# Kernel optimization log

Hardware: AMD Instinct MI355X
Metric: run time of the kernel (lower is better)

## Reference

```python
import jax, jax.numpy as jnp
import numpy as np

B, N, DIM = 8, 1024, 512
HEADS, DIM_HEAD = 8, 64
INNER = HEADS * DIM_HEAD  # 512
SCALE = DIM_HEAD ** -0.5
EPS = 1e-5


def setup_inputs() -> dict:
    key = jax.random.key(0)
    k = jax.random.split(key, 6)
    x = jax.random.normal(k[0], (B, N, DIM), dtype=jnp.float32)
    gamma = jnp.ones((DIM,), dtype=jnp.float32)
    beta = jnp.zeros((DIM,), dtype=jnp.float32)
    # Linear weights stored as (in, out) so y = x @ W (equivalent to torch x @ W.T)
    W_qk = jax.random.normal(k[1], (DIM, 2 * INNER), dtype=jnp.float32) * (DIM ** -0.5)
    W_v = jax.random.normal(k[2], (DIM, INNER), dtype=jnp.float32) * (DIM ** -0.5)
    W_out = jax.random.normal(k[3], (INNER, DIM), dtype=jnp.float32) * (INNER ** -0.5)
    return {"x": x, "gamma": gamma, "beta": beta, "W_qk": W_qk, "W_v": W_v, "W_out": W_out}


def _layernorm(x, gamma, beta):
    mu = jnp.mean(x, axis=-1, keepdims=True)
    var = jnp.mean(jnp.square(x - mu), axis=-1, keepdims=True)
    return (x - mu) * jax.lax.rsqrt(var + EPS) * gamma + beta


def reference(x, gamma, beta, W_qk, W_v, W_out):
    xn = _layernorm(x, gamma, beta)                       # [B,N,D]
    v = xn @ W_v                                          # [B,N,INNER]
    qk = xn @ W_qk                                        # [B,N,2*INNER]
    q, k = jnp.split(qk, 2, axis=-1)
    # b n (h d) -> b h n d
    q = q.reshape(B, N, HEADS, DIM_HEAD).transpose(0, 2, 1, 3)
    k = k.reshape(B, N, HEADS, DIM_HEAD).transpose(0, 2, 1, 3)
    vh = v.reshape(B, N, HEADS, DIM_HEAD).transpose(0, 2, 1, 3)
    dots = jnp.einsum('bhnd,bhmd->bhnm', q, k) * SCALE    # [B,H,N,N]
    attn = jax.nn.softmax(dots, axis=-1)
    out = jnp.einsum('bhnm,bhmd->bhnd', attn, vh)         # [B,H,N,d]
    out = out.transpose(0, 2, 1, 3).reshape(B, N, INNER)  # b h n d -> b n (h d)
    return out @ W_out                                    # [B,N,DIM]
```

## Files before the change

### kernel.cpp

```cpp
#include <hip/hip_runtime.h>

#define TOK 8192
#define DMODEL 512
#define SEQ 1024
#define NH 8
#define DH 64

typedef _Float16 half8 __attribute__((ext_vector_type(8)));
typedef _Float16 half4v __attribute__((ext_vector_type(4)));
typedef float floatx4 __attribute__((ext_vector_type(4)));

__device__ __forceinline__ void gll16(const void* g, void* l) {
  __builtin_amdgcn_global_load_lds(
      (const __attribute__((address_space(1))) void*)g,
      (__attribute__((address_space(3))) void*)l, 16, 0, 0);
}

__global__ __launch_bounds__(256) void ln_kernel(
    const float* __restrict__ x, const float* __restrict__ gamma,
    const float* __restrict__ beta, _Float16* __restrict__ xn) {
  const int row = blockIdx.x * 4 + (threadIdx.x >> 6);
  const int t = threadIdx.x & 63;
  const float* xr = x + (size_t)row * DMODEL;
  const float4 a = *(const float4*)(xr + t * 4);
  const float4 b = *(const float4*)(xr + 256 + t * 4);
  float s  = a.x + a.y + a.z + a.w + b.x + b.y + b.z + b.w;
  float ss = a.x*a.x + a.y*a.y + a.z*a.z + a.w*a.w
           + b.x*b.x + b.y*b.y + b.z*b.z + b.w*b.w;
  #pragma unroll
  for (int m = 1; m < 64; m <<= 1) {
    s  += __shfl_xor(s, m);
    ss += __shfl_xor(ss, m);
  }
  const float mean = s * (1.0f / DMODEL);
  const float var  = ss * (1.0f / DMODEL) - mean * mean;
  const float inv  = rsqrtf(var + 1e-5f);
  const float4 g0  = *(const float4*)(gamma + t * 4);
  const float4 g1  = *(const float4*)(gamma + 256 + t * 4);
  const float4 be0 = *(const float4*)(beta + t * 4);
  const float4 be1 = *(const float4*)(beta + 256 + t * 4);
  half4v o0, o1;
  o0[0] = (_Float16)((a.x - mean) * inv * g0.x + be0.x);
  o0[1] = (_Float16)((a.y - mean) * inv * g0.y + be0.y);
  o0[2] = (_Float16)((a.z - mean) * inv * g0.z + be0.z);
  o0[3] = (_Float16)((a.w - mean) * inv * g0.w + be0.w);
  o1[0] = (_Float16)((b.x - mean) * inv * g1.x + be1.x);
  o1[1] = (_Float16)((b.y - mean) * inv * g1.y + be1.y);
  o1[2] = (_Float16)((b.z - mean) * inv * g1.z + be1.z);
  o1[3] = (_Float16)((b.w - mean) * inv * g1.w + be1.w);
  _Float16* outr = xn + (size_t)row * DMODEL;
  *(half4v*)(outr + t * 4) = o0;
  *(half4v*)(outr + 256 + t * 4) = o1;
}

__global__ __launch_bounds__(256) void transpose_cvt3_kernel(
    const float* __restrict__ Wqk, const float* __restrict__ Wv,
    const float* __restrict__ Wo, _Float16* __restrict__ WqkvT,
    _Float16* __restrict__ WoutT) {
  const int z = blockIdx.z;
  const float* W;
  _Float16* dst;
  int N, rowoff;
  if (z == 0)      { W = Wqk; dst = WqkvT; N = 1024; rowoff = 0; }
  else if (z == 1) { W = Wv;  dst = WqkvT; N = 512;  rowoff = 1024; }
  else             { W = Wo;  dst = WoutT; N = 512;  rowoff = 0; }
  const int n0 = blockIdx.x * 32;
  if (n0 >= N) return;
  const int k0 = blockIdx.y * 32;
  __shared__ float t[32][33];
  const int tx = threadIdx.x & 31, ty = threadIdx.x >> 5;
  #pragma unroll
  for (int j = 0; j < 4; ++j)
    t[ty + j * 8][tx] = W[(size_t)(k0 + ty + j * 8) * N + n0 + tx];
  __syncthreads();
  #pragma unroll
  for (int j = 0; j < 4; ++j)
    dst[(size_t)(rowoff + n0 + ty + j * 8) * 512 + k0 + tx] =
        (_Float16)t[tx][ty + j * 8];
}

template <int MODE>
__global__ __launch_bounds__(256) void hgemm_kernel(
    const _Float16* __restrict__ A, const _Float16* __restrict__ Bt,
    void* __restrict__ Cout, void* __restrict__ Cout2, int M, int N, int K) {
  __shared__ char smem[65536];
  const int tid = threadIdx.x;
  const int bm = blockIdx.x, bn = blockIdx.y;
  const int wv = tid >> 6, lane = tid & 63;
  const int l15 = lane & 15, g = lane >> 4;
  const int wr = wv >> 1, wc = wv & 1;
  const int swz = (l15 & 7) << 4;
  const _Float16* Ab = A + (size_t)(bm * 128) * K;
  const _Float16* Bb = Bt + (size_t)(bn * 128) * K;
  const int lrow = lane >> 3;
  const int lchk = (lane & 7) * 16;
  const int ssw = lchk ^ (lrow << 4);

  #define HG_STAGE(buf, kt)                                                  \
    _Pragma("unroll")                                                        \
    for (int i = 0; i < 4; ++i) {                                            \
      const int row = wv * 32 + i * 8 + lrow;                                \
      gll16((const char*)(Ab + (size_t)row * K + (kt)) + ssw,                \
            smem + (buf) * 32768 + (wv * 32 + i * 8) * 128);                 \
      gll16((const char*)(Bb + (size_t)row * K + (kt)) + ssw,                \
            smem + (buf) * 32768 + 16384 + (wv * 32 + i * 8) * 128);         \
    }

  floatx4 acc[4][4] = {};
  HG_STAGE(0, 0);
  __syncthreads();
  int cur = 0;
  for (int kt = 0; kt < K; kt += 64) {
    if (kt + 64 < K) { HG_STAGE(cur ^ 1, kt + 64); }
    const char* sb = smem + cur * 32768;
    #pragma unroll
    for (int kk = 0; kk < 2; ++kk) {
      half8 af[4], bf[4];
      #pragma unroll
      for (int mt = 0; mt < 4; ++mt)
        af[mt] = *(const half8*)(sb + (wr * 64 + mt * 16 + l15) * 128 +
                                 ((g * 16 + kk * 64) ^ swz));
      #pragma unroll
      for (int nt = 0; nt < 4; ++nt)
        bf[nt] = *(const half8*)(sb + 16384 + (wc * 64 + nt * 16 + l15) * 128 +
                                 ((g * 16 + kk * 64) ^ swz));
      #pragma unroll
      for (int mt = 0; mt < 4; ++mt)
        #pragma unroll
        for (int nt = 0; nt < 4; ++nt)
          acc[mt][nt] = __builtin_amdgcn_mfma_f32_16x16x32_f16(
              af[mt], bf[nt], acc[mt][nt], 0, 0, 0);
    }
    __syncthreads();
    cur ^= 1;
  }
  #undef HG_STAGE
  const int m0 = bm * 128 + wr * 64;
  const int n0 = bn * 128 + wc * 64;
  if constexpr (MODE == 0) {
    float* C = (float*)Cout;
    #pragma unroll
    for (int mt = 0; mt < 4; ++mt)
      #pragma unroll
      for (int nt = 0; nt < 4; ++nt) {
        const int n = n0 + nt * 16 + l15;
        #pragma unroll
        for (int r = 0; r < 4; ++r)
          C[(size_t)(m0 + mt * 16 + 4 * g + r) * 512 + n] = acc[mt][nt][r];
      }
  } else {
    _Float16* Q = (_Float16*)Cout;
    _Float16* V = (_Float16*)Cout2;
    #pragma unroll
    for (int mt = 0; mt < 4; ++mt) {
      const int mrow = m0 + mt * 16 + 4 * g;
      const int b = mrow >> 10, tok = mrow & 1023;
      #pragma unroll
      for (int nt = 0; nt < 4; ++nt) {
        const int n = n0 + nt * 16 + l15;
        if (n < 1024) {
          #pragma unroll
          for (int r = 0; r < 4; ++r)
            Q[(size_t)(mrow + r) * 1024 + n] = (_Float16)acc[mt][nt][r];
        } else {
          const int cv = n - 1024;
          half4v hv;
          #pragma unroll
          for (int r = 0; r < 4; ++r) hv[r] = (_Float16)acc[mt][nt][r];
          *(half4v*)(V + ((size_t)((b * 8 + (cv >> 6)) * 64 + (cv & 63)) << 10) + tok) = hv;
        }
      }
    }
  }
}

#define QSC 0.18033688f
#define MOFF 5.7707801f

__global__ __launch_bounds__(512) void flash16_kernel(
    const _Float16* __restrict__ qkh, const _Float16* __restrict__ vt,
    _Float16* __restrict__ ao) {
  __shared__ char smem[65536];
  const int bh = blockIdx.x;
  const int qt = blockIdx.y;
  const int b = bh >> 3, h = bh & 7;
  const int tid = threadIdx.x;
  const int wv = tid >> 6, lane = tid & 63;
  const int l15 = lane & 15, g = lane >> 4;
  const int swz = (l15 & 7) << 4;
  const int qrow0 = b * SEQ + qt * 128;

  half8 qf[2];
  {
    const _Float16* qp = qkh + (size_t)(qrow0 + wv * 16 + l15) * 1024 + h * DH;
    qf[0] = *(const half8*)(qp + g * 8);
    qf[1] = *(const half8*)(qp + g * 8 + 32);
    qf[0] *= (_Float16)QSC;
    qf[1] *= (_Float16)QSC;
  }

  float lsum = 0.f;
  floatx4 oacc[4] = {};

  const int lrow = lane >> 3;
  const int lchk = (lane & 7) * 16;
  const int ssw = lchk ^ (lrow << 4);
  const _Float16* kbase = qkh + 512 + h * DH;
  const _Float16* vbase = vt + (size_t)bh * 64 * 1024;
  char* pb = smem + 49152 + wv * 2048 + l15 * 128;

  #define FL_STAGE(buf, kt)                                                   \
    {                                                                         \
      const int krow = b * SEQ + (kt) * 64 + wv * 8 + lrow;                   \
      gll16((const char*)(kbase + (size_t)krow * 1024) + ssw,                 \
            smem + (buf) * 16384 + wv * 1024);                                \
      gll16((const char*)(vbase + (size_t)(wv * 8 + lrow) * 1024 +            \
                          (kt) * 64) + ssw,                                   \
            smem + (buf) * 16384 + 8192 + wv * 1024);                         \
    }

  FL_STAGE(0, 0);
  FL_STAGE(1, 1);
  int cur = 0;
  for (int kt = 0; kt < 16; ++kt) {
    if (kt < 15) asm volatile("s_waitcnt vmcnt(2)" ::: "memory");
    else         asm volatile("s_waitcnt vmcnt(0)" ::: "memory");
    __builtin_amdgcn_s_barrier();
    asm volatile("" ::: "memory");
    const int nxt = cur + 2 >= 3 ? cur - 1 : cur + 2;
    if (kt + 2 < 16) FL_STAGE(nxt, kt + 2);
    const char* sb = smem + cur * 16384;

    floatx4 sacc[4] = {};
    __builtin_amdgcn_s_setprio(1);
    #pragma unroll
    for (int kk = 0; kk < 2; ++kk) {
      #pragma unroll
      for (int mt = 0; mt < 4; ++mt) {
        half8 af = *(const half8*)(sb + (16 * mt + l15) * 128 +
                                   ((g * 16 + kk * 64) ^ swz));
        sacc[mt] = __builtin_amdgcn_mfma_f32_16x16x32_f16(af, qf[kk], sacc[mt], 0, 0, 0);
      }
    }
    __builtin_amdgcn_s_setprio(0);

    float rs = 0.f;
    #pragma unroll
    for (int mt = 0; mt < 4; ++mt) {
      float p0 = exp2f(sacc[mt][0] - MOFF);
      float p1 = exp2f(sacc[mt][1] - MOFF);
      float p2 = exp2f(sacc[mt][2] - MOFF);
      float p3 = exp2f(sacc[mt][3] - MOFF);
      rs += (p0 + p1) + (p2 + p3);
      half4v pv;
      pv[0] = (_Float16)p0; pv[1] = (_Float16)p1;
      pv[2] = (_Float16)p2; pv[3] = (_Float16)p3;
      *(half4v*)(pb + ((32 * mt + 8 * g) ^ swz)) = pv;
    }
    rs += __shfl_xor(rs, 16);
    rs += __shfl_xor(rs, 32);
    lsum += rs;

    __builtin_amdgcn_s_setprio(1);
    #pragma unroll
    for (int kk = 0; kk < 2; ++kk) {
      half8 pf = *(const half8*)(pb + ((g * 16 + kk * 64) ^ swz));
      #pragma unroll
      for (int mt = 0; mt < 4; ++mt) {
        half8 vf = *(const half8*)(sb + 8192 + (16 * mt + l15) * 128 +
                                   ((g * 16 + kk * 64) ^ swz));
        oacc[mt] = __builtin_amdgcn_mfma_f32_16x16x32_f16(vf, pf, oacc[mt], 0, 0, 0);
      }
    }
    __builtin_amdgcn_s_setprio(0);
    cur = cur + 1 >= 3 ? 0 : cur + 1;
  }
  #undef FL_STAGE

  const float inv = 1.0f / lsum;
  _Float16* op = ao + (size_t)(qrow0 + wv * 16 + l15) * 512 + h * DH;
  #pragma unroll
  for (int mt = 0; mt < 4; ++mt) {
    half4v hv;
    hv[0] = (_Float16)(oacc[mt][0] * inv);
    hv[1] = (_Float16)(oacc[mt][1] * inv);
    hv[2] = (_Float16)(oacc[mt][2] * inv);
    hv[3] = (_Float16)(oacc[mt][3] * inv);
    *(half4v*)(op + 16 * mt + 4 * g) = hv;
  }
}

extern "C" void kernel_launch(void* const* d_in, const int* in_sizes, int n_in,
                              void* d_out, int out_size, void* d_ws, size_t ws_size,
                              hipStream_t stream) {
  const float* x     = (const float*)d_in[0];
  const float* gamma = (const float*)d_in[1];
  const float* beta  = (const float*)d_in[2];
  const float* W_qk  = (const float*)d_in[3];
  const float* W_v   = (const float*)d_in[4];
  const float* W_out = (const float*)d_in[5];
  float* out = (float*)d_out;
  char* ws = (char*)d_ws;

  const size_t MB = 1024 * 1024;
  _Float16* xn16  = (_Float16*)ws;
  _Float16* qkh   = (_Float16*)(ws + 8 * MB);
  _Float16* vt    = (_Float16*)(ws + 24 * MB);
  _Float16* ao16  = (_Float16*)(ws + 32 * MB);
  _Float16* WqkvT = (_Float16*)(ws + 40 * MB);
  _Float16* WoutT = (_Float16*)(ws + 42 * MB);

  transpose_cvt3_kernel<<<dim3(32, 16, 3), 256, 0, stream>>>(
      W_qk, W_v, W_out, WqkvT, WoutT);
  ln_kernel<<<TOK / 4, 256, 0, stream>>>(x, gamma, beta, xn16);
  hgemm_kernel<3><<<dim3(64, 12), 256, 0, stream>>>(
      xn16, WqkvT, qkh, vt, TOK, 1536, 512);
  flash16_kernel<<<dim3(64, 8), 512, 0, stream>>>(qkh, vt, ao16);
  hgemm_kernel<0><<<dim3(64, 4), 256, 0, stream>>>(
      ao16, WoutT, out, nullptr, TOK, 512, 512);
}
```

Baseline: 81.90 us.

## Merge LN and weight transpose kernels; triple-buffer GEMM with BK=32 pipeline

Merges the layernorm kernel and the weight transpose/convert kernel into one launch that picks its role from the block index, removing one kernel launch. Reworks the GEMM main loop from a double-buffered 64-wide K tile into a three-stage ring of 32-wide K tiles. Loads are issued two stages ahead and waited on with explicit vmcnt counts and a raw barrier, and MFMA priority is raised during compute. LDS drops to 48KB, which may allow more blocks per CU, at the cost of more barriers per K step and a new swizzle pattern.

```diff
diff --git a/kernel.cpp b/kernel.cpp
--- a/kernel.cpp
+++ b/kernel.cpp
@@ -16,123 +16,130 @@
       (__attribute__((address_space(3))) void*)l, 16, 0, 0);
 }
 
-__global__ __launch_bounds__(256) void ln_kernel(
+__global__ __launch_bounds__(256) void prep_kernel(
     const float* __restrict__ x, const float* __restrict__ gamma,
-    const float* __restrict__ beta, _Float16* __restrict__ xn) {
-  const int row = blockIdx.x * 4 + (threadIdx.x >> 6);
-  const int t = threadIdx.x & 63;
-  const float* xr = x + (size_t)row * DMODEL;
-  const float4 a = *(const float4*)(xr + t * 4);
-  const float4 b = *(const float4*)(xr + 256 + t * 4);
-  float s  = a.x + a.y + a.z + a.w + b.x + b.y + b.z + b.w;
-  float ss = a.x*a.x + a.y*a.y + a.z*a.z + a.w*a.w
-           + b.x*b.x + b.y*b.y + b.z*b.z + b.w*b.w;
-  #pragma unroll
-  for (int m = 1; m < 64; m <<= 1) {
-    s  += __shfl_xor(s, m);
-    ss += __shfl_xor(ss, m);
-  }
-  const float mean = s * (1.0f / DMODEL);
-  const float var  = ss * (1.0f / DMODEL) - mean * mean;
-  const float inv  = rsqrtf(var + 1e-5f);
-  const float4 g0  = *(const float4*)(gamma + t * 4);
-  const float4 g1  = *(const float4*)(gamma + 256 + t * 4);
-  const float4 be0 = *(const float4*)(beta + t * 4);
-  const float4 be1 = *(const float4*)(beta + 256 + t * 4);
-  half4v o0, o1;
-  o0[0] = (_Float16)((a.x - mean) * inv * g0.x + be0.x);
-  o0[1] = (_Float16)((a.y - mean) * inv * g0.y + be0.y);
-  o0[2] = (_Float16)((a.z - mean) * inv * g0.z + be0.z);
-  o0[3] = (_Float16)((a.w - mean) * inv * g0.w + be0.w);
-  o1[0] = (_Float16)((b.x - mean) * inv * g1.x + be1.x);
-  o1[1] = (_Float16)((b.y - mean) * inv * g1.y + be1.y);
-  o1[2] = (_Float16)((b.z - mean) * inv * g1.z + be1.z);
-  o1[3] = (_Float16)((b.w - mean) * inv * g1.w + be1.w);
-  _Float16* outr = xn + (size_t)row * DMODEL;
-  *(half4v*)(outr + t * 4) = o0;
-  *(half4v*)(outr + 256 + t * 4) = o1;
-}
-
-__global__ __launch_bounds__(256) void transpose_cvt3_kernel(
+    const float* __restrict__ beta, _Float16* __restrict__ xn,
     const float* __restrict__ Wqk, const float* __restrict__ Wv,
     const float* __restrict__ Wo, _Float16* __restrict__ WqkvT,
     _Float16* __restrict__ WoutT) {
-  const int z = blockIdx.z;
-  const float* W;
-  _Float16* dst;
-  int N, rowoff;
-  if (z == 0)      { W = Wqk; dst = WqkvT; N = 1024; rowoff = 0; }
-  else if (z == 1) { W = Wv;  dst = WqkvT; N = 512;  rowoff = 1024; }
-  else             { W = Wo;  dst = WoutT; N = 512;  rowoff = 0; }
-  const int n0 = blockIdx.x * 32;
-  if (n0 >= N) return;
-  const int k0 = blockIdx.y * 32;
   __shared__ float t[32][33];
-  const int tx = threadIdx.x & 31, ty = threadIdx.x >> 5;
-  #pragma unroll
-  for (int j = 0; j < 4; ++j)
-    t[ty + j * 8][tx] = W[(size_t)(k0 + ty + j * 8) * N + n0 + tx];
-  __syncthreads();
-  #pragma unroll
-  for (int j = 0; j < 4; ++j)
-    dst[(size_t)(rowoff + n0 + ty + j * 8) * 512 + k0 + tx] =
-        (_Float16)t[tx][ty + j * 8];
+  const int bid = blockIdx.x;
+  if (bid < 2048) {
+    const int row = bid * 4 + (threadIdx.x >> 6);
+    const int tt = threadIdx.x & 63;
+    const float* xr = x + (size_t)row * DMODEL;
+    const float4 a = *(const float4*)(xr + tt * 4);
+    const float4 b = *(const float4*)(xr + 256 + tt * 4);
+    float s  = a.x + a.y + a.z + a.w + b.x + b.y + b.z + b.w;
+    float ss = a.x*a.x + a.y*a.y + a.z*a.z + a.w*a.w
+             + b.x*b.x + b.y*b.y + b.z*b.z + b.w*b.w;
+    #pragma unroll
+    for (int m = 1; m < 64; m <<= 1) {
+      s  += __shfl_xor(s, m);
+      ss += __shfl_xor(ss, m);
+    }
+    const float mean = s * (1.0f / DMODEL);
+    const float var  = ss * (1.0f / DMODEL) - mean * mean;
+    const float inv  = rsqrtf(var + 1e-5f);
+    const float4 g0  = *(const float4*)(gamma + tt * 4);
+    const float4 g1  = *(const float4*)(gamma + 256 + tt * 4);
+    const float4 be0 = *(const float4*)(beta + tt * 4);
+    const float4 be1 = *(const float4*)(beta + 256 + tt * 4);
+    half4v o0, o1;
+    o0[0] = (_Float16)((a.x - mean) * inv * g0.x + be0.x);
+    o0[1] = (_Float16)((a.y - mean) * inv * g0.y + be0.y);
+    o0[2] = (_Float16)((a.z - mean) * inv * g0.z + be0.z);
+    o0[3] = (_Float16)((a.w - mean) * inv * g0.w + be0.w);
+    o1[0] = (_Float16)((b.x - mean) * inv * g1.x + be1.x);
+    o1[1] = (_Float16)((b.y - mean) * inv * g1.y + be1.y);
+    o1[2] = (_Float16)((b.z - mean) * inv * g1.z + be1.z);
+    o1[3] = (_Float16)((b.w - mean) * inv * g1.w + be1.w);
+    _Float16* outr = xn + (size_t)row * DMODEL;
+    *(half4v*)(outr + tt * 4) = o0;
+    *(half4v*)(outr + 256 + tt * 4) = o1;
+  } else {
+    const int r = bid - 2048;
+    const int z = r >> 9;
+    const int rem = r & 511;
+    const float* W;
+    _Float16* dst;
+    int N, rowoff;
+    if (z == 0)      { W = Wqk; dst = WqkvT; N = 1024; rowoff = 0; }
+    else if (z == 1) { W = Wv;  dst = WqkvT; N = 512;  rowoff = 1024; }
+    else             { W = Wo;  dst = WoutT; N = 512;  rowoff = 0; }
+    const int n0 = (rem & 31) * 32;
+    if (n0 >= N) return;
+    const int k0 = (rem >> 5) * 32;
+    const int tx = threadIdx.x & 31, ty = threadIdx.x >> 5;
+    #pragma unroll
+    for (int j = 0; j < 4; ++j)
+      t[ty + j * 8][tx] = W[(size_t)(k0 + ty + j * 8) * N + n0 + tx];
+    __syncthreads();
+    #pragma unroll
+    for (int j = 0; j < 4; ++j)
+      dst[(size_t)(rowoff + n0 + ty + j * 8) * 512 + k0 + tx] =
+          (_Float16)t[tx][ty + j * 8];
+  }
 }
 
 template <int MODE>
 __global__ __launch_bounds__(256) void hgemm_kernel(
     const _Float16* __restrict__ A, const _Float16* __restrict__ Bt,
     void* __restrict__ Cout, void* __restrict__ Cout2, int M, int N, int K) {
-  __shared__ char smem[65536];
+  __shared__ char smem[49152];
   const int tid = threadIdx.x;
   const int bm = blockIdx.x, bn = blockIdx.y;
   const int wv = tid >> 6, lane = tid & 63;
   const int l15 = lane & 15, g = lane >> 4;
   const int wr = wv >> 1, wc = wv & 1;
-  const int swz = (l15 & 7) << 4;
+  const int rswz = ((l15 >> 1) & 3) << 4;
   const _Float16* Ab = A + (size_t)(bm * 128) * K;
   const _Float16* Bb = Bt + (size_t)(bn * 128) * K;
-  const int lrow = lane >> 3;
-  const int lchk = (lane & 7) * 16;
-  const int ssw = lchk ^ (lrow << 4);
-
-  #define HG_STAGE(buf, kt)                                                  \
-    _Pragma("unroll")                                                        \
-    for (int i = 0; i < 4; ++i) {                                            \
-      const int row = wv * 32 + i * 8 + lrow;                                \
-      gll16((const char*)(Ab + (size_t)row * K + (kt)) + ssw,                \
-            smem + (buf) * 32768 + (wv * 32 + i * 8) * 128);                 \
-      gll16((const char*)(Bb + (size_t)row * K + (kt)) + ssw,                \
-            smem + (buf) * 32768 + 16384 + (wv * 32 + i * 8) * 128);         \
+  const int lrow = lane >> 2;
+  const int lchk = (lane & 3) * 16;
+  const int ssw = lchk ^ (((lrow >> 1) & 3) << 4);
+
+  #define HG_STAGE(buf, kt)                                                   \
+    _Pragma("unroll")                                                         \
+    for (int i = 0; i < 2; ++i) {                                             \
+      const int rbase = wv * 16 + i * 64;                                     \
+      gll16((const char*)(Ab + (size_t)(rbase + lrow) * K + (kt)) + ssw,      \
+            smem + (buf) * 16384 + rbase * 64);                               \
+      gll16((const char*)(Bb + (size_t)(rbase + lrow) * K + (kt)) + ssw,      \
+            smem + (buf) * 16384 + 8192 + rbase * 64);                        \
     }
 
   floatx4 acc[4][4] = {};
   HG_STAGE(0, 0);
-  __syncthreads();
+  HG_STAGE(1, 32);
   int cur = 0;
-  for (int kt = 0; kt < K; kt += 64) {
-    if (kt + 64 < K) { HG_STAGE(cur ^ 1, kt + 64); }
-    const char* sb = smem + cur * 32768;
-    #pragma unroll
-    for (int kk = 0; kk < 2; ++kk) {
-      half8 af[4], bf[4];
-      #pragma unroll
-      for (int mt = 0; mt < 4; ++mt)
-        af[mt] = *(const half8*)(sb + (wr * 64 + mt * 16 + l15) * 128 +
-                                 ((g * 16 + kk * 64) ^ swz));
+  const int nit = K >> 5;
+  for (int it = 0; it < nit; ++it) {
+    if (it < nit - 2) asm volatile("s_waitcnt vmcnt(4)" ::: "memory");
+    else              asm volatile("s_waitcnt vmcnt(0)" ::: "memory");
+    __builtin_amdgcn_s_barrier();
+    asm volatile("" ::: "memory");
+    const int nxt = cur + 2 >= 3 ? cur - 1 : cur + 2;
+    if (it + 2 < nit) { HG_STAGE(nxt, (it + 2) * 32); }
+    const char* sb = smem + cur * 16384;
+    half8 af[4], bf[4];
+    #pragma unroll
+    for (int mt = 0; mt < 4; ++mt)
+      af[mt] = *(const half8*)(sb + (wr * 64 + mt * 16 + l15) * 64 +
+                               (g * 16 ^ rswz));
+    #pragma unroll
+    for (int nt = 0; nt < 4; ++nt)
+      bf[nt] = *(const half8*)(sb + 8192 + (wc * 64 + nt * 16 + l15) * 64 +
+                               (g * 16 ^ rswz));
+    __builtin_amdgcn_s_setprio(1);
+    #pragma unroll
+    for (int mt = 0; mt < 4; ++mt)
       #pragma unroll
       for (int nt = 0; nt < 4; ++nt)
-        bf[nt] = *(const half8*)(sb + 16384 + (wc * 64 + nt * 16 + l15) * 128 +
-                                 ((g * 16 + kk * 64) ^ swz));
-      #pragma unroll
-      for (int mt = 0; mt < 4; ++mt)
-        #pragma unroll
-        for (int nt = 0; nt < 4; ++nt)
-          acc[mt][nt] = __builtin_amdgcn_mfma_f32_16x16x32_f16(
-              af[mt], bf[nt], acc[mt][nt], 0, 0, 0);
-    }
-    __syncthreads();
-    cur ^= 1;
+        acc[mt][nt] = __builtin_amdgcn_mfma_f32_16x16x32_f16(
+            af[mt], bf[nt], acc[mt][nt], 0, 0, 0);
+    __builtin_amdgcn_s_setprio(0);
+    cur = cur + 1 >= 3 ? 0 : cur + 1;
   }
   #undef HG_STAGE
   const int m0 = bm * 128 + wr * 64;
@@ -310,9 +317,8 @@
   _Float16* WqkvT = (_Float16*)(ws + 40 * MB);
   _Float16* WoutT = (_Float16*)(ws + 42 * MB);
 
-  transpose_cvt3_kernel<<<dim3(32, 16, 3), 256, 0, stream>>>(
-      W_qk, W_v, W_out, WqkvT, WoutT);
-  ln_kernel<<<TOK / 4, 256, 0, stream>>>(x, gamma, beta, xn16);
+  prep_kernel<<<3584, 256, 0, stream>>>(x, gamma, beta, xn16,
+                                        W_qk, W_v, W_out, WqkvT, WoutT);
   hgemm_kernel<3><<<dim3(64, 12), 256, 0, stream>>>(
       xn16, WqkvT, qkh, vt, TOK, 1536, 512);
   flash16_kernel<<<dim3(64, 8), 512, 0, stream>>>(qkh, vt, ao16);
```

Result: faster. 74.45 us (-9.1%).
